# Kernel tuning notes

Measured on AMD Instinct MI355X. Metric: run time of the kernel, lower is better.

## Reference

```python
import jax, jax.numpy as jnp
import numpy as np

OLD_W, OLD_H = 224, 224   # raster image spatial size (originalShape[2:])
NEW_W, NEW_H = 28, 28     # feature-grid spatial size (newShape[2:])
B, N_SV, HID = 64, 63, 512  # batch, surrounding agents (N-1), LSTM encoder hidden
POS_SCALE = 250.0         # some positions exceed OLD_W to exercise validity masks


def setup_inputs() -> dict:
    key = jax.random.key(0)
    k1, k2, k3 = jax.random.split(key, 3)
    svPositionsAtT0 = jax.random.uniform(k1, (B, N_SV, 3), dtype=jnp.float32) * POS_SCALE
    svEncoding = jax.random.normal(k2, (B, N_SV, HID), dtype=jnp.float32)
    lengths = jax.random.randint(k3, (B,), 0, N_SV, dtype=jnp.int32)
    return {"svPositionsAtT0": svPositionsAtT0, "svEncoding": svEncoding, "lengths": lengths}


def reference(svPositionsAtT0, svEncoding, lengths):
    # Faithful vectorized form of rawToRasterScaleSocialState:
    # sequential per-agent max-writes into a zero-initialized grid == scatter-max.
    b_, n_, hid = svEncoding.shape
    x = svPositionsAtT0[..., 0]                     # (B, N)
    y = svPositionsAtT0[..., 1]
    xIdx = (x * NEW_W / OLD_W).astype(jnp.int32)    # trunc toward zero, as .long()
    yIdx = (y * NEW_H / OLD_H).astype(jnp.int32)
    agent_ids = jnp.arange(n_, dtype=lengths.dtype)[None, :]
    mask = (lengths[:, None] > agent_ids) & (xIdx < NEW_W) & (yIdx < NEW_H)  # (B, N)
    # Invalid agents: write 0 (no-op since grid init is 0 and writes are max-with-0)
    enc = jnp.where(mask[..., None], svEncoding, 0.0)          # (B, N, HID)
    xI = jnp.clip(xIdx, 0, NEW_W - 1)
    yI = jnp.clip(yIdx, 0, NEW_H - 1)
    bI = jnp.broadcast_to(jnp.arange(b_)[:, None], (b_, n_))
    grid = jnp.zeros((b_, hid, NEW_W, NEW_H), dtype=svEncoding.dtype)
    grid = grid.at[bI.ravel(), :, xI.ravel(), yI.ravel()].max(enc.reshape(b_ * n_, hid))
    return grid
```

## Files before the change

kernel.cpp:

```cpp
#include <hip/hip_runtime.h>
#include <hip/hip_bf16.h>

#define NSV    63
#define HID    512
#define GW     28
#define GH     28
#define CELLS  (GW * GH)
#define HCHUNK 16
#define NTHREADS 256

__global__ __launch_bounds__(NTHREADS)
void scatter_grid_kernel(const float* __restrict__ pos,
                         const float* __restrict__ enc,
                         const int*   __restrict__ lengths,
                         float*       __restrict__ out) {
    const int b      = blockIdx.y;
    const int h_base = blockIdx.x * HCHUNK;
    const int t      = threadIdx.x;

    __shared__ int   cell_s[NSV];
    __shared__ float enc_s[NSV * HCHUNK];
    __shared__ float grid_s[HCHUNK * CELLS];

    if (t < NSV) {
        const float x = pos[((size_t)b * NSV + t) * 3 + 0];
        const float y = pos[((size_t)b * NSV + t) * 3 + 1];
        const int len = lengths[b];
        const int xi = (int)(x * 28.0f / 224.0f);
        const int yi = (int)(y * 28.0f / 224.0f);
        const bool valid = (t < len) && (xi < GW) && (yi < GH);
        const int xc = min(max(xi, 0), GW - 1);
        const int yc = min(max(yi, 0), GH - 1);
        cell_s[t] = valid ? (xc * GH + yc) : -1;
    }

    {
        const int n = t >> 2;
        const int q = t & 3;
        if (n < NSV) {
            const float4 v = ((const float4*)(enc + ((size_t)b * NSV + n) * HID + h_base))[q];
            ((float4*)(enc_s + n * HCHUNK))[q] = v;
        }
    }

    {
        float4* g4 = (float4*)grid_s;
        const float4 z = make_float4(0.f, 0.f, 0.f, 0.f);
        #pragma unroll
        for (int i = t; i < HCHUNK * CELLS / 4; i += NTHREADS) g4[i] = z;
    }
    __syncthreads();

    {
        const int h    = t >> 4;
        const int part = t & 15;
        float* row = grid_s + h * CELLS;
        #pragma unroll
        for (int n = 0; n < NSV; ++n) {
            const int c = cell_s[n];
            if (c >= 0 && (c & 15) == part) {
                const float v = enc_s[n * HCHUNK + h];
                if (v > row[c]) row[c] = v;
            }
        }
    }
    __syncthreads();

    {
        float* outb = out + ((size_t)b * HID + h_base) * CELLS;
        const float4* s4 = (const float4*)grid_s;
        float4* d4 = (float4*)outb;
        #pragma unroll
        for (int i = t; i < HCHUNK * CELLS / 4; i += NTHREADS) d4[i] = s4[i];
    }
}

extern "C" void kernel_launch(void* const* d_in, const int* in_sizes, int n_in,
                              void* d_out, int out_size, void* d_ws, size_t ws_size,
                              hipStream_t stream) {
    const float* pos     = (const float*)d_in[0];
    const float* enc     = (const float*)d_in[1];
    const int*   lengths = (const int*)d_in[2];
    float*       out     = (float*)d_out;

    const int B = in_sizes[2];

    dim3 grid(HID / HCHUNK, B);
    dim3 block(NTHREADS);
    scatter_grid_kernel<<<grid, block, 0, stream>>>(pos, enc, lengths, out);
}
```

Baseline: 132.6 us.

## Replace shared grid scatter with per-cell agent bitmasks and gather on output

```diff
diff --git a/kernel.cpp b/kernel.cpp
--- a/kernel.cpp
+++ b/kernel.cpp
@@ -8,6 +8,8 @@
 #define CELLS  (GW * GH)
 #define HCHUNK 16
 #define NTHREADS 256
+#define NF4    (HCHUNK * CELLS / 4)
+#define F4ROW  (CELLS / 4)
 
 __global__ __launch_bounds__(NTHREADS)
 void scatter_grid_kernel(const float* __restrict__ pos,
@@ -18,21 +20,10 @@
     const int h_base = blockIdx.x * HCHUNK;
     const int t      = threadIdx.x;
 
-    __shared__ int   cell_s[NSV];
+    __shared__ unsigned long long mask_s[CELLS];
     __shared__ float enc_s[NSV * HCHUNK];
-    __shared__ float grid_s[HCHUNK * CELLS];
 
-    if (t < NSV) {
-        const float x = pos[((size_t)b * NSV + t) * 3 + 0];
-        const float y = pos[((size_t)b * NSV + t) * 3 + 1];
-        const int len = lengths[b];
-        const int xi = (int)(x * 28.0f / 224.0f);
-        const int yi = (int)(y * 28.0f / 224.0f);
-        const bool valid = (t < len) && (xi < GW) && (yi < GH);
-        const int xc = min(max(xi, 0), GW - 1);
-        const int yc = min(max(yi, 0), GH - 1);
-        cell_s[t] = valid ? (xc * GH + yc) : -1;
-    }
+    for (int c = t; c < CELLS; c += NTHREADS) mask_s[c] = 0ull;
 
     {
         const int n = t >> 2;
@@ -42,36 +33,39 @@
             ((float4*)(enc_s + n * HCHUNK))[q] = v;
         }
     }
-
-    {
-        float4* g4 = (float4*)grid_s;
-        const float4 z = make_float4(0.f, 0.f, 0.f, 0.f);
-        #pragma unroll
-        for (int i = t; i < HCHUNK * CELLS / 4; i += NTHREADS) g4[i] = z;
-    }
     __syncthreads();
 
-    {
-        const int h    = t >> 4;
-        const int part = t & 15;
-        float* row = grid_s + h * CELLS;
-        #pragma unroll
-        for (int n = 0; n < NSV; ++n) {
-            const int c = cell_s[n];
-            if (c >= 0 && (c & 15) == part) {
-                const float v = enc_s[n * HCHUNK + h];
-                if (v > row[c]) row[c] = v;
-            }
+    if (t < NSV) {
+        const float x = pos[((size_t)b * NSV + t) * 3 + 0];
+        const float y = pos[((size_t)b * NSV + t) * 3 + 1];
+        const int len = lengths[b];
+        const int xi = (int)(x * 28.0f / 224.0f);
+        const int yi = (int)(y * 28.0f / 224.0f);
+        if ((t < len) && (xi < GW) && (yi < GH)) {
+            const int xc = min(max(xi, 0), GW - 1);
+            const int yc = min(max(yi, 0), GH - 1);
+            atomicOr(&mask_s[xc * GH + yc], 1ull << t);
         }
     }
     __syncthreads();
 
-    {
-        float* outb = out + ((size_t)b * HID + h_base) * CELLS;
-        const float4* s4 = (const float4*)grid_s;
-        float4* d4 = (float4*)outb;
+    float4* d4 = (float4*)(out + ((size_t)b * HID + h_base) * CELLS);
+    for (int i = t; i < NF4; i += NTHREADS) {
+        const int h = i / F4ROW;
+        const int c = (i - h * F4ROW) * 4;
+        float4 v = make_float4(0.f, 0.f, 0.f, 0.f);
         #pragma unroll
-        for (int i = t; i < HCHUNK * CELLS / 4; i += NTHREADS) d4[i] = s4[i];
+        for (int j = 0; j < 4; ++j) {
+            unsigned long long m = mask_s[c + j];
+            float val = 0.f;
+            while (m) {
+                const int n = __ffsll(m) - 1;
+                m &= m - 1;
+                val = fmaxf(val, enc_s[n * HCHUNK + h]);
+            }
+            (&v.x)[j] = val;
+        }
+        d4[i] = v;
     }
 }
 
```

Result: faster. 118.7 us (-10.5%).
